# Optimization experiments

Measured on AMD Instinct MI355X. Metric: run time of the kernel, lower is better.

## Reference

```python
import jax, jax.numpy as jnp
import numpy as np
from jax import lax

IMG = 1280.0          # image side (80 * stride 16)
HF = WF = 80          # feature map
STRIDE = 16
A = 15                # anchors per location (5 sizes x 3 ratios)
KMIX = 5              # MDN mixture components
NIMG = 8
NGT = 32
PRE_NMS = 2000
POST_NMS = 1000
NMS_THRESH = 0.7
BATCH_PER_IMG = 256
POS_FRAC = 0.5
SCALE_CLAMP = float(np.log(1000.0 / 16.0))
LOG2PI = float(np.log(2.0 * np.pi))


def _make_anchors():
    sizes = np.array([32., 64., 128., 256., 512.])
    ratios = np.array([0.5, 1.0, 2.0])
    ws = (sizes[:, None] * np.sqrt(1.0 / ratios)[None, :]).reshape(-1)
    hs = (sizes[:, None] * np.sqrt(ratios)[None, :]).reshape(-1)
    base = np.stack([-ws / 2, -hs / 2, ws / 2, hs / 2], 1)  # [A,4]
    xs = (np.arange(WF) + 0.5) * STRIDE
    ys = (np.arange(HF) + 0.5) * STRIDE
    sx, sy = np.meshgrid(xs, ys)
    shifts = np.stack([sx.ravel(), sy.ravel(), sx.ravel(), sy.ravel()], 1)  # [HW,4]
    return jnp.asarray((shifts[:, None, :] + base[None]).reshape(-1, 4), jnp.float32)


def setup_inputs() -> dict:
    key = jax.random.key(0)
    k = jax.random.split(key, 6)
    R = HF * WF * A
    anchors = _make_anchors()                                                # [R,4]
    pi = jax.random.normal(k[0], (NIMG, KMIX, R), jnp.float32)
    mu = jax.random.normal(k[1], (NIMG, KMIX, R), jnp.float32)
    sigma = jax.random.uniform(k[2], (NIMG, KMIX, R), jnp.float32, 0.1, 1.0)
    deltas = jax.random.normal(k[3], (NIMG, R, 4), jnp.float32) * 0.1
    xy = jax.random.uniform(k[4], (NIMG, NGT, 2), jnp.float32, 0.0, 960.0)
    wh = jax.random.uniform(k[5], (NIMG, NGT, 2), jnp.float32, 20.0, 320.0)
    gt_boxes = jnp.concatenate([xy, xy + wh], -1)                            # [N,G,4]
    return {"anchors": anchors, "pi": pi, "mu": mu, "sigma": sigma,
            "deltas": deltas, "gt_boxes": gt_boxes}


def pairwise_iou(a, b):  # [M,4],[P,4] -> [M,P]
    area_a = (a[:, 2] - a[:, 0]) * (a[:, 3] - a[:, 1])
    area_b = (b[:, 2] - b[:, 0]) * (b[:, 3] - b[:, 1])
    lt = jnp.maximum(a[:, None, :2], b[None, :, :2])
    rb = jnp.minimum(a[:, None, 2:], b[None, :, 2:])
    wh = jnp.clip(rb - lt, 0.0)
    inter = wh[..., 0] * wh[..., 1]
    return inter / jnp.maximum(area_a[:, None] + area_b[None, :] - inter, 1e-9)


def apply_deltas(d, boxes):  # Box2BoxTransform.apply_deltas, weights=(1,1,1,1)
    w = boxes[:, 2] - boxes[:, 0]
    h = boxes[:, 3] - boxes[:, 1]
    cx = boxes[:, 0] + 0.5 * w
    cy = boxes[:, 1] + 0.5 * h
    dx, dy = d[:, 0], d[:, 1]
    dw = jnp.minimum(d[:, 2], SCALE_CLAMP)
    dh = jnp.minimum(d[:, 3], SCALE_CLAMP)
    pcx = dx * w + cx
    pcy = dy * h + cy
    pw = jnp.exp(dw) * w
    ph = jnp.exp(dh) * h
    return jnp.stack([pcx - 0.5 * pw, pcy - 0.5 * ph, pcx + 0.5 * pw, pcy + 0.5 * ph], 1)


def get_deltas(src, tgt):  # Box2BoxTransform.get_deltas
    sw = src[..., 2] - src[..., 0]
    sh = src[..., 3] - src[..., 1]
    scx = src[..., 0] + 0.5 * sw
    scy = src[..., 1] + 0.5 * sh
    tw = tgt[..., 2] - tgt[..., 0]
    th = tgt[..., 3] - tgt[..., 1]
    tcx = tgt[..., 0] + 0.5 * tw
    tcy = tgt[..., 1] + 0.5 * th
    return jnp.stack([(tcx - scx) / sw, (tcy - scy) / sh,
                      jnp.log(tw / sw), jnp.log(th / sh)], -1)


def _nms_image(boxes, scores, unc):  # [R,4],[R],[R,2] -> padded top proposals
    top_s, tidx = lax.top_k(scores, PRE_NMS)
    tb = jnp.clip(boxes[tidx], 0.0, IMG)   # clip to image
    tu = unc[tidx]
    iou = pairwise_iou(tb, tb)             # [PRE,PRE]
    ar = jnp.arange(PRE_NMS)

    def body(i, keep):
        sup = (iou[i] > NMS_THRESH) & (ar > i) & keep[i]
        return keep & ~sup

    keep = lax.fori_loop(0, PRE_NMS, body, jnp.ones((PRE_NMS,), bool))
    wv = tb[:, 2] - tb[:, 0]
    hv = tb[:, 3] - tb[:, 1]
    keep = keep & (wv > 0.0) & (hv > 0.0)  # min_box_size = 0
    ms = jnp.where(keep, top_s, -jnp.inf)
    out_s, oidx = lax.top_k(ms, POST_NMS)
    return tb[oidx], out_s, tu[oidx]


def _losses(anchors, pi, mu, sigma, deltas, gt_boxes):
    # label_and_sample_anchors (no_grad in torch)
    iou = lax.stop_gradient(jax.vmap(lambda g: pairwise_iou(g, anchors))(gt_boxes))  # [N,G,R]
    vals = iou.max(axis=1)                       # matched IoU quality  [N,R]
    idx = jnp.argmax(iou, axis=1)                # matched gt index     [N,R]
    labels = jnp.where(vals >= 0.7, 1, jnp.where(vals >= 0.3, -1, 0))
    best_gt = iou.max(axis=2)                    # [N,G]
    lq = jnp.any((iou >= best_gt[:, :, None] - 1e-7) & (best_gt[:, :, None] > 0), axis=1)
    labels = jnp.where(lq, 1, labels)            # allow_low_quality_matches
    # deterministic subsample to batch_size_per_image with positive_fraction
    pos = labels == 1
    neg = labels == 0
    n_pos = jnp.minimum(pos.sum(1), int(BATCH_PER_IMG * POS_FRAC))
    keep_pos = pos & (jnp.cumsum(pos, 1) <= n_pos[:, None])
    keep_neg = neg & (jnp.cumsum(neg, 1) <= (BATCH_PER_IMG - n_pos)[:, None])
    labels = jnp.where(keep_pos, 1, jnp.where(keep_neg, 0, -1))
    matched_gt = lax.stop_gradient(jax.vmap(lambda g, i: g[i])(gt_boxes, idx))  # [N,R,4]
    gt_deltas = get_deltas(lax.stop_gradient(anchors)[None], matched_gt)
    pos_mask = labels == 1
    # smooth_l1 with beta=0 -> L1, summed over positives
    loss_loc = jnp.sum(jnp.abs(deltas - gt_deltas) * pos_mask[..., None])
    valid = labels != -1
    t = jnp.clip(vals, 0.0, 1.0)
    lp = jax.nn.log_softmax(pi, axis=1)
    comp = lp - 0.5 * ((t[:, None, :] - mu) / sigma) ** 2 - jnp.log(sigma) - 0.5 * LOG2PI
    nll = -jax.nn.logsumexp(comp, axis=1)        # [N,R]
    loss_cls = jnp.sum(nll * valid)
    norm = BATCH_PER_IMG * pi.shape[0]
    return jnp.stack([loss_cls / norm, loss_loc / norm])


def reference(anchors, pi, mu, sigma, deltas, gt_boxes):
    # find_logit: pi-weighted mixture mean as objectness score
    pi_sm = jax.nn.softmax(pi, axis=1)           # [N,K,R]
    logits = jnp.sum(pi_sm * mu, axis=1)         # [N,R]
    # mdn_uncertainties: epistemic / aleatoric
    epis = jnp.sum(pi_sm * (mu - logits[:, None, :]) ** 2, axis=1)
    alea = jnp.sum(pi_sm * sigma ** 2, axis=1)
    unc = jnp.stack([epis, alea], -1)            # [N,R,2]
    # _decode_proposals
    boxes = jax.vmap(lambda d: apply_deltas(d, anchors))(deltas)  # [N,R,4]
    # find_top_rpn_proposals_uncertainty (pre-NMS topk, clip, NMS, post-NMS topk)
    prop_b, prop_s, prop_u = jax.vmap(_nms_image)(boxes, logits, unc)
    losses = _losses(anchors, pi, mu, sigma, deltas, gt_boxes)    # [loss_cls, loss_loc]
    return prop_b, prop_s, prop_u, losses
```

## Files before the change

### kernel.cpp

```cpp
#include <hip/hip_runtime.h>
#include <cstdint>
#include <cstddef>

typedef unsigned long long u64;
typedef unsigned int u32;
typedef unsigned short u16;
typedef unsigned char u8;

#define R_ANCH 96000
#define NIMG   8
#define KMIX   5
#define PRE    2000
#define POST   1000
#define NGT    32
#define NCHUNK 375
#define NBLK   48
#define MROW   2048
#define GC_STRIDE 16
#define SCAP   16
#define BIG_TH 64

#define IMG_SZ        1280.0f
#define NMS_T         0.7f
#define SCALE_CLAMP_F 4.135166556742356f
#define HALF_L2PI     0.9189385332046727f

__device__ __forceinline__ u64 make_key(float s, int r) {
  u32 u = __float_as_uint(s);
  u = (u & 0x80000000u) ? ~u : (u | 0x80000000u);
  return ((u64)u << 32) | (u64)(0xFFFFFFFFu - (u32)r);
}

__device__ __forceinline__ float dec_score(u64 key) {
  u32 o = (u32)(key >> 32);
  u32 bits = (o & 0x80000000u) ? (o ^ 0x80000000u) : ~o;
  return __uint_as_float(bits);
}

__device__ __forceinline__ float iou_pair(float a0,float a1,float a2,float a3,
                                          float b0,float b1,float b2,float b3) {
#pragma clang fp contract(off)
  float areaA = (a2-a0)*(a3-a1);
  float areaB = (b2-b0)*(b3-b1);
  float lx=fmaxf(a0,b0), ly=fmaxf(a1,b1);
  float rx=fminf(a2,b2), ry=fminf(a3,b3);
  float iw=fmaxf(rx-lx,0.0f), ih=fmaxf(ry-ly,0.0f);
  float inter=iw*ih;
  return inter / fmaxf(areaA+areaB-inter, 1e-9f);
}

__device__ __forceinline__ void pick2048(const u32* __restrict__ hist, int k,
                                         int* s_i, u32* s_u,
                                         int& d_out, int& k_out, u32& cnt_out) {
  int tid = threadIdx.x;
  int lane = tid & 63, w = tid >> 6;
  u32 h[8]; u32 ssum = 0;
#pragma unroll
  for (int i=0;i<8;++i){ h[i] = hist[2047 - (tid*8 + i)]; ssum += h[i]; }
  u32 incl = ssum;
  for (int off=1; off<64; off<<=1){
    u32 t = (u32)__shfl_up((int)incl, off, 64);
    if (lane >= off) incl += t;
  }
  if (lane==63) s_i[w] = (int)incl;
  __syncthreads();
  u32 base = 0;
  for (int ww=0; ww<w; ++ww) base += (u32)s_i[ww];
  u32 run = base + incl - ssum;
#pragma unroll
  for (int i=0;i<8;++i){
    u32 nr = run + h[i];
    if (run < (u32)k && nr >= (u32)k){
      s_u[0] = (u32)(2047 - (tid*8+i));
      s_u[1] = (u32)k - run;
      s_u[2] = h[i];
    }
    run = nr;
  }
  __syncthreads();
  d_out = (int)s_u[0]; k_out = (int)s_u[1]; cnt_out = s_u[2];
  __syncthreads();
}

__device__ __forceinline__ void scan2048_desc(const u32* __restrict__ h,
                                              u32* __restrict__ off,
                                              u32* __restrict__ wsum, int tid) {
  int b_hi = 2047 - 2*tid, b_lo = b_hi - 1;
  u32 h_hi = h[b_hi], h_lo = h[b_lo];
  u32 sum = h_hi + h_lo;
  u32 incl = sum;
  int lane = tid & 63, wv = tid >> 6;
  for (int o=1; o<64; o<<=1){
    u32 t = (u32)__shfl_up((int)incl, o, 64);
    if (lane >= o) incl += t;
  }
  if (lane==63) wsum[wv] = incl;
  __syncthreads();
  u32 base = 0;
  for (int w=0; w<wv; ++w) base += wsum[w];
  u32 excl = base + incl - sum;
  off[b_hi] = excl;
  off[b_lo] = excl + h_hi;
}

__global__ void kZero(u32* z, int nwords) {
  for (int i = blockIdx.x*256 + threadIdx.x; i < nwords; i += gridDim.x*256)
    z[i] = 0u;
}

__global__ __launch_bounds__(256) void kA_mdn(
    const float* __restrict__ pi, const float* __restrict__ mu,
    const float* __restrict__ sigma, float* __restrict__ logits,
    float* __restrict__ epis, float* __restrict__ alea,
    u32* __restrict__ hist0,
    const float* __restrict__ anchors, const float* __restrict__ gt,
    const float* __restrict__ deltas,
    float* __restrict__ nll_o, float* __restrict__ loc_o) {
  __shared__ u32 s_h[2048];
  __shared__ float s_gt[NGT*4];
  int tid = threadIdx.x;
  int r = blockIdx.x*256 + tid;
  int img = blockIdx.y;
  for (int b=tid; b<2048; b+=256) s_h[b]=0u;
  if (tid < NGT*4) s_gt[tid] = gt[img*NGT*4 + tid];
  size_t base = (size_t)img*KMIX*R_ANCH + r;
  float p[KMIX], m[KMIX], s[KMIX];
#pragma unroll
  for (int k=0;k<KMIX;k++){
    p[k]=pi[base+(size_t)k*R_ANCH];
    m[k]=mu[base+(size_t)k*R_ANCH];
    s[k]=sigma[base+(size_t)k*R_ANCH];
  }
  float mx = p[0];
#pragma unroll
  for (int k=1;k<KMIX;k++) mx = fmaxf(mx,p[k]);
  float e[KMIX]; float sum = 0.0f;
#pragma unroll
  for (int k=0;k<KMIX;k++){ e[k]=expf(p[k]-mx); sum += e[k]; }
  float w[KMIX]; float lg = 0.0f;
#pragma unroll
  for (int k=0;k<KMIX;k++){ w[k]=e[k]/sum; lg += w[k]*m[k]; }
  float ep = 0.0f, al = 0.0f;
#pragma unroll
  for (int k=0;k<KMIX;k++){ float d=m[k]-lg; ep += w[k]*d*d; al += w[k]*s[k]*s[k]; }
  size_t o = (size_t)img*R_ANCH + r;
  logits[o]=lg; epis[o]=ep; alea[o]=al;
  __syncthreads();
  u64 key = make_key(lg, r);
  atomicAdd(&s_h[(u32)(key>>53)], 1u);
  float4 a = ((const float4*)anchors)[r];
  float aA = (a.z-a.x)*(a.w-a.y);
  float bi = -1.0f, bu = 1.0f; int idx = 0;
#pragma unroll 4
  for (int g=0; g<NGT; ++g){
    float g0=s_gt[g*4], g1=s_gt[g*4+1], g2=s_gt[g*4+2], g3=s_gt[g*4+3];
    float ga=(g2-g0)*(g3-g1);
    float lx=fmaxf(g0,a.x), ly=fmaxf(g1,a.y);
    float rx=fminf(g2,a.z), ry=fminf(g3,a.w);
    float iw=fmaxf(rx-lx,0.0f), ih=fmaxf(ry-ly,0.0f);
    float inter=iw*ih;
    float uni = fmaxf(ga + aA - inter, 1e-9f);
    if (inter*bu > bi*uni){ bi=inter; bu=uni; idx=g; }
  }
  float vbest = bi/bu;
  float lsum = logf(sum);
  float t_ = fminf(fmaxf(vbest, 0.0f), 1.0f);
  float comp[KMIX];
#pragma unroll
  for (int k=0;k<KMIX;k++){
    float z = (t_ - m[k]) / s[k];
    comp[k] = (p[k]-mx-lsum) - 0.5f*z*z - logf(s[k]) - HALF_L2PI;
  }
  float cm = comp[0];
#pragma unroll
  for (int k=1;k<KMIX;k++) cm = fmaxf(cm, comp[k]);
  float se = 0.0f;
#pragma unroll
  for (int k=0;k<KMIX;k++) se += expf(comp[k]-cm);
  float nll = -(cm + logf(se));
  const float* gb = &s_gt[idx*4];
  float sw = a.z-a.x, sh = a.w-a.y;
  float scx = a.x+0.5f*sw, scy = a.y+0.5f*sh;
  float tw = gb[2]-gb[0], th = gb[3]-gb[1];
  float tcx = gb[0]+0.5f*tw, tcy = gb[1]+0.5f*th;
  float4 d = ((const float4*)deltas)[(size_t)img*R_ANCH + r];
  float loc = fabsf(d.x-(tcx-scx)/sw) + fabsf(d.y-(tcy-scy)/sh)
            + fabsf(d.z-logf(tw/sw)) + fabsf(d.w-logf(th/sh));
  nll_o[o] = nll; loc_o[o] = loc;
  __syncthreads();
  for (int b=tid; b<2048; b+=256){ u32 v=s_h[b]; if(v) atomicAdd(&hist0[img*2048+b], v); }
}

__global__ __launch_bounds__(256) void kL1_bestgt(const float* __restrict__ anchors,
                                                  const float* __restrict__ gt,
                                                  int* __restrict__ best) {
  __shared__ float s_gt[NGT*4];
  __shared__ float s_ga[NGT];
  __shared__ int s_best[NGT];
  int tid = threadIdx.x, img = blockIdx.y;
  if (tid < NGT*4) s_gt[tid] = gt[img*NGT*4 + tid];
  if (tid < NGT){
    const float* g4 = gt + img*NGT*4 + tid*4;
    s_ga[tid] = (g4[2]-g4[0])*(g4[3]-g4[1]);
    s_best[tid] = 0;
  }
  __syncthreads();
  float4 an[8]; float aA[8];
#pragma unroll
  for (int q=0; q<8; ++q){
    int r = blockIdx.x*256 + tid + q*(NBLK*256);
    an[q] = (r < R_ANCH) ? ((const float4*)anchors)[r]
                         : make_float4(0.f,0.f,0.f,0.f);
    aA[q] = (an[q].z-an[q].x)*(an[q].w-an[q].y);
  }
  float vmax[NGT];
#pragma unroll 2
  for (int g=0; g<NGT; ++g){
    float g0=s_gt[g*4], g1=s_gt[g*4+1], g2=s_gt[g*4+2], g3=s_gt[g*4+3];
    float ga=s_ga[g];
    float bi=0.0f, bu=1.0f;
#pragma unroll
    for (int q=0; q<8; ++q){
      float lx=fmaxf(g0,an[q].x), ly=fmaxf(g1,an[q].y);
      float rx=fminf(g2,an[q].z), ry=fminf(g3,an[q].w);
      float iw=fmaxf(rx-lx,0.0f), ih=fmaxf(ry-ly,0.0f);
      float inter=iw*ih;
      float uni=fmaxf(ga+aA[q]-inter,1e-9f);
      if (inter*bu > bi*uni){ bi=inter; bu=uni; }
    }
    vmax[g] = bi/bu;
  }
  int lane = tid & 63;
#pragma unroll
  for (int g=0; g<NGT; ++g){
    float v = vmax[g];
    v = fmaxf(v, __shfl_xor(v, 1, 64));
    v = fmaxf(v, __shfl_xor(v, 2, 64));
    v = fmaxf(v, __shfl_xor(v, 4, 64));
    v = fmaxf(v, __shfl_xor(v, 8, 64));
    v = fmaxf(v, __shfl_xor(v,16, 64));
    v = fmaxf(v, __shfl_xor(v,32, 64));
    if (lane==0 && v > 0.0f) atomicMax(&s_best[g], __float_as_int(v));
  }
  __syncthreads();
  if (tid < NGT) atomicMax(&best[img*NGT + tid], s_best[tid]);
}

__global__ __launch_bounds__(256) void kP1(const float* __restrict__ logits,
                                           const u32* __restrict__ hist0,
                                           u32* __restrict__ hist1) {
  __shared__ u32 s_h[2048];
  __shared__ int s_i[8]; __shared__ u32 s_u[3];
  int img = blockIdx.y, tid = threadIdx.x;
  int d0,k0; u32 c0;
  pick2048(hist0 + img*2048, PRE, s_i, s_u, d0,k0,c0);
  if (c0 <= 2048u) return;
  for (int b=tid; b<2048; b+=256) s_h[b]=0u;
  __syncthreads();
  const float* sc = logits + (size_t)img*R_ANCH;
  for (int r = blockIdx.x*256 + tid; r < R_ANCH; r += NBLK*256){
    u64 key = make_key(sc[r], r);
    if ((int)(key>>53) == d0) atomicAdd(&s_h[(u32)(key>>42)&2047u], 1u);
  }
  __syncthreads();
  for (int b=tid; b<2048; b+=256){ u32 v=s_h[b]; if(v) atomicAdd(&hist1[img*2048+b], v); }
}

__global__ __launch_bounds__(256) void kP2(const float* __restrict__ logits,
                                           const u32* __restrict__ hist0,
                                           const u32* __restrict__ hist1,
                                           u32* __restrict__ hist2) {
  __shared__ u32 s_h[2048];
  __shared__ int s_i[8]; __shared__ u32 s_u[3];
  int img = blockIdx.y, tid = threadIdx.x;
  int d0,k0; u32 c0;
  pick2048(hist0 + img*2048, PRE, s_i, s_u, d0,k0,c0);
  if (c0 <= 2048u) return;
  int d1,k1; u32 c1;
  pick2048(hist1 + img*2048, k0, s_i, s_u, d1,k1,c1);
  if (c1 <= 2048u) return;
  u64 p1 = ((u64)d0<<11) | (u64)d1;
  for (int b=tid; b<2048; b+=256) s_h[b]=0u;
  __syncthreads();
  const float* sc = logits + (size_t)img*R_ANCH;
  for (int r = blockIdx.x*256 + tid; r < R_ANCH; r += NBLK*256){
    u64 key = make_key(sc[r], r);
    if ((key>>42) == p1) atomicAdd(&s_h[(u32)(key>>31)&2047u], 1u);
  }
  __syncthreads();
  for (int b=tid; b<2048; b+=256){ u32 v=s_h[b]; if(v) atomicAdd(&hist2[img*2048+b], v); }
}

__global__ __launch_bounds__(256) void kGather(const float* __restrict__ logits,
    const u32* __restrict__ hist0, const u32* __restrict__ hist1,
    const u32* __restrict__ hist2, u64* __restrict__ cand, u32* __restrict__ gcnt) {
  __shared__ int s_i[8]; __shared__ u32 s_u[3];
  __shared__ u64 s_cand[2048];
  __shared__ u32 s_cnt, s_base;
  int img = blockIdx.y, tid = threadIdx.x;
  if (tid==0) s_cnt = 0u;
  int d,kk; u32 c;
  pick2048(hist0 + img*2048, PRE, s_i, s_u, d,kk,c);
  u64 p = (u64)d; int L = 0;
  if (c > 2048u){
    pick2048(hist1 + img*2048, kk, s_i, s_u, d,kk,c);
    p = (p<<11)|(u64)d; L = 1;
    if (c > 2048u){
      pick2048(hist2 + img*2048, kk, s_i, s_u, d,kk,c);
      p = (p<<11)|(u64)d; L = 2;
    }
  }
  u64 T = p << (64 - 11*(L+1));
  const float* sc = logits + (size_t)img*R_ANCH;
  int lane = tid & 63;
  for (int r = blockIdx.x*256 + tid; r < R_ANCH; r += NBLK*256){
    u64 key = make_key(sc[r], r);
    bool take = (key >= T);
    u64 b = __ballot(take);
    if (b){
      u32 base = 0;
      if (lane==0) base = atomicAdd(&s_cnt, (u32)__popcll(b));
      base = (u32)__shfl((int)base, 0, 64);
      if (take){
        u32 pos = base + (u32)__popcll(b & ((1ull<<lane)-1ull));
        if (pos < 2048u) s_cand[pos] = key;
        else {
          u32 gp = atomicAdd(&gcnt[img*GC_STRIDE], 1u);
          if (gp < 4096u) cand[(size_t)img*4096 + gp] = key;
        }
      }
    }
  }
  __syncthreads();
  u32 n = s_cnt < 2048u ? s_cnt : 2048u;
  if (tid==0) s_base = atomicAdd(&gcnt[img*GC_STRIDE], n);
  __syncthreads();
  u32 gb = s_base;
  for (u32 i=tid; i<n; i+=256)
    cand[(size_t)img*4096 + gb + i] = s_cand[i];
}

__global__ __launch_bounds__(1024) void kRank(
    const u64* __restrict__ cand, const u32* __restrict__ gcnt,
    const float* __restrict__ epis, const float* __restrict__ alea,
    const float* __restrict__ deltas, const float* __restrict__ anchors,
    float* __restrict__ tb, float* __restrict__ tu, float* __restrict__ ts) {
  __shared__ u64 s_key[4096];
  __shared__ u16 s_idx0[4096];
  __shared__ u16 s_idx1[4096];
  __shared__ u32 s_h0[2048];
  __shared__ u32 s_off0[2048];
  __shared__ u32 s_h1[2048];
  __shared__ u32 s_off1[2048];
  __shared__ u32 s_wsum[16];
  __shared__ u32 s_nbig;
  __shared__ u16 s_big[64];
  int tid = threadIdx.x, img = blockIdx.x;
  u32 cnt = gcnt[img*GC_STRIDE];
  if (cnt > 4096u) cnt = 4096u;
  const u64* cp = cand + (size_t)img*4096;
  for (int i=tid; i<4096; i+=1024) s_key[i] = (i < (int)cnt) ? cp[i] : 0ull;
  for (int b=tid; b<2048; b+=1024){ s_h0[b] = 0u; }
  if (tid==0) s_nbig = 0u;
  __syncthreads();
  for (int i=tid; i<(int)cnt; i+=1024)
    atomicAdd(&s_h0[(u32)(s_key[i]>>53)], 1u);
  __syncthreads();
  scan2048_desc(s_h0, s_off0, s_wsum, tid);
  __syncthreads();
  for (int b=tid; b<2048; b+=1024){
    u32 sz = s_h0[b];
    if (sz > BIG_TH && s_off0[b] < PRE){
      u32 q = atomicAdd(&s_nbig, 1u);
      if (q < 64u) s_big[q] = (u16)b;
    }
  }
  for (int i=tid; i<(int)cnt; i+=1024){
    u32 d = (u32)(s_key[i]>>53);
    u32 slot = atomicAdd(&s_off0[d], 1u);
    s_idx0[slot] = (u16)i;
  }
  __syncthreads();
  auto emit = [&](u64 my, u32 rank){
    if (rank < PRE){
      int p = (int)rank;
      u32 idx = 0xFFFFFFFFu - (u32)(my & 0xFFFFFFFFull);
      ts[img*PRE + p] = dec_score(my);
      float4 a = ((const float4*)anchors)[idx];
      float4 dd = ((const float4*)deltas)[(size_t)img*R_ANCH + idx];
      float w = a.z - a.x, h = a.w - a.y;
      float cx = a.x + 0.5f*w, cy = a.y + 0.5f*h;
      float dw = fminf(dd.z, SCALE_CLAMP_F), dh = fminf(dd.w, SCALE_CLAMP_F);
      float pcx = dd.x*w + cx, pcy = dd.y*h + cy;
      float pw = expf(dw)*w, ph = expf(dh)*h;
      float x0 = fminf(fmaxf(pcx - 0.5f*pw, 0.0f), IMG_SZ);
      float y0 = fminf(fmaxf(pcy - 0.5f*ph, 0.0f), IMG_SZ);
      float x1 = fminf(fmaxf(pcx + 0.5f*pw, 0.0f), IMG_SZ);
      float y1 = fminf(fmaxf(pcy + 0.5f*ph, 0.0f), IMG_SZ);
      ((float4*)tb)[(size_t)img*PRE + p] = make_float4(x0,y0,x1,y1);
      size_t o = (size_t)img*R_ANCH + idx;
      ((float2*)tu)[(size_t)img*PRE + p] = make_float2(epis[o], alea[o]);
    }
  };
  for (int i=tid; i<(int)cnt; i+=1024){
    u64 my = s_key[i];
    u32 d = (u32)(my>>53);
    u32 size = s_h0[d];
    if (size > BIG_TH) continue;
    u32 bs = s_off0[d] - size;
    if (bs >= PRE) continue;
    u32 rank = bs;
    for (u32 q=bs; q<bs+size; ++q)
      rank += (s_key[s_idx0[q]] > my) ? 1u : 0u;
    emit(my, rank);
  }
  __syncthreads();
  u32 nbig = s_nbig < 64u ? s_nbig : 64u;
  for (u32 bb=0; bb<nbig; ++bb){
    u32 B = s_big[bb];
    u32 size = s_h0[B];
    u32 base0 = s_off0[B] - size;
    for (int b=tid; b<2048; b+=1024) s_h1[b] = 0u;
    __syncthreads();
    for (u32 q=tid; q<size; q+=1024){
      u64 k = s_key[s_idx0[base0+q]];
      atomicAdd(&s_h1[(u32)(k>>42)&2047u], 1u);
    }
    __syncthreads();
    scan2048_desc(s_h1, s_off1, s_wsum, tid);
    __syncthreads();
    for (u32 q=tid; q<size; q+=1024){
      u16 ci = s_idx0[base0+q];
      u64 k = s_key[ci];
      u32 slot = atomicAdd(&s_off1[(u32)(k>>42)&2047u], 1u);
      s_idx1[slot] = ci;
    }
    __syncthreads();
    for (u32 q=tid; q<size; q+=1024){
      u16 ci = s_idx1[q];
      u64 my = s_key[ci];
      u32 d1 = (u32)(my>>42)&2047u;
      u32 ssz = s_h1[d1];
      u32 sbs = s_off1[d1] - ssz;
      u32 rank = base0 + sbs;
      for (u32 t2=sbs; t2<sbs+ssz; ++t2)
        rank += (s_key[s_idx1[t2]] > my) ? 1u : 0u;
      emit(my, rank);
    }
    __syncthreads();
  }
}

__global__ __launch_bounds__(1024) void kD_mask(const float* __restrict__ tb,
                                                u64* __restrict__ maskLT,
                                                u32* __restrict__ scnt,
                                                u16* __restrict__ slist) {
  __shared__ float4 s_tile[64];
  int tid = threadIdx.x;
  int a = blockIdx.x, img = blockIdx.y;
  const float4* tbi = (const float4*)tb + (size_t)img*PRE;
  if (tid < 64){
    int i = a*64 + tid;
    s_tile[tid] = (i < PRE) ? tbi[i] : make_float4(0.f,0.f,0.f,0.f);
  }
  __syncthreads();
  u64* outp = maskLT + ((size_t)img*32 + a)*MROW;
  u32* cnts = scnt + (size_t)img*2048;
  u16* lst  = slist + (size_t)img*2048*SCAP;
  int bmax = min(64, PRE - a*64);
  for (int j = a*64 + tid; j < MROW; j += 1024){
    u64 m = 0ull;
    if (j < PRE){
      float4 B = tbi[j];
      int blim = min(bmax, j - a*64);
      for (int b = 0; b < blim; ++b){
        float4 A = s_tile[b];
        float v = iou_pair(A.x,A.y,A.z,A.w, B.x,B.y,B.z,B.w);
        m |= (u64)(v > NMS_T) << b;
      }
    }
    outp[j] = m;
    u64 mm = m;
    while (mm){
      int b = __builtin_ctzll(mm); mm &= mm - 1ull;
      u32 slot = atomicAdd(&cnts[j], 1u);
      if (slot < SCAP) lst[(size_t)j*SCAP + slot] = (u16)(a*64 + b);
    }
  }
}

__global__ __launch_bounds__(1024) void kE_nms(const u64* __restrict__ maskLT,
                                               const u32* __restrict__ scnt,
                                               const u16* __restrict__ slist,
                                               u64* __restrict__ keep) {
  __shared__ u64 s_list64[2048*SCAP/4];
  __shared__ u16 s_cnt[2048];
  __shared__ u8  kbuf[2][2048];
  __shared__ u64 s_kw[32];
  __shared__ int s_change, s_ovf;
  int img = blockIdx.x, tid = threadIdx.x;
  const u64* gl = (const u64*)(slist + (size_t)img*2048*SCAP);
  for (int i=tid; i<2048*SCAP/4; i+=1024) s_list64[i] = gl[i];
  const u32* gc = scnt + (size_t)img*2048;
  for (int i=tid; i<2048; i+=1024) s_cnt[i] = (u16)gc[i];
  if (tid==0){ s_change = 0; s_ovf = 0; }
  __syncthreads();
  bool myovf = false;
#pragma unroll
  for (int q=0; q<2; ++q){
    int j = tid + q*1024;
    if (s_cnt[j] > SCAP) myovf = true;
    kbuf[0][j] = (j < PRE) ? 1 : 0;
  }
  if (myovf) s_ovf = 1;
  __syncthreads();
  const u64* MT = maskLT + (size_t)img*32*MROW;
  int cur = 0;
  for (int iter=0; iter<2048; ++iter){
    bool ovf = (s_ovf != 0);
    if (ovf && tid < 32){
      u64 w = 0ull;
      for (int b=0; b<64; ++b) w |= (u64)(kbuf[cur][tid*64+b] & 1) << b;
      s_kw[tid] = w;
    }
    __syncthreads();
    bool changed = false;
#pragma unroll
    for (int q=0; q<2; ++q){
      int j = tid + q*1024;
      u8 old = kbuf[cur][j];
      u8 nk = (j < PRE) ? 1 : 0;
      if (nk){
        int cnt = s_cnt[j];
        if (cnt <= SCAP){
          const u16* lp = (const u16*)&s_list64[j*(SCAP/4)];
          for (int i=0; i<cnt; ++i){
            if (kbuf[cur][lp[i]]){ nk = 0; break; }
          }
        } else {
          int amax = j >> 6;
          for (int a=0; a<=amax; ++a){
            if (MT[(size_t)a*MROW + j] & s_kw[a]){ nk = 0; break; }
          }
        }
      }
      kbuf[1-cur][j] = nk;
      changed |= (nk != old);
    }
    if (changed) s_change = 1;
    __syncthreads();
    int ch = s_change;
    __syncthreads();
    if (tid==0) s_change = 0;
    if (!ch) break;
    cur ^= 1;
  }
  if (tid < 32){
    u64 w = 0ull;
    for (int b=0; b<64; ++b) w |= (u64)(kbuf[cur][tid*64+b] & 1) << b;
    keep[img*32 + tid] = w;
  }
}

__global__ __launch_bounds__(256) void kL2_label(
    const float* __restrict__ anchors, const float* __restrict__ gt,
    const int* __restrict__ best,
    signed char* __restrict__ label, int* __restrict__ cpos, int* __restrict__ cneg) {
  __shared__ float s_gt[NGT*4];
  __shared__ float s_ga[NGT];
  __shared__ float s_bg[NGT];
  __shared__ int s_w[8];
  int tid = threadIdx.x, img = blockIdx.y;
  int r = blockIdx.x*256 + tid;
  if (tid < NGT*4) s_gt[tid] = gt[img*NGT*4 + tid];
  if (tid < NGT){
    const float* g4 = gt + img*NGT*4 + tid*4;
    s_ga[tid] = (g4[2]-g4[0])*(g4[3]-g4[1]);
    s_bg[tid] = __int_as_float(best[img*NGT + tid]);
  }
  __syncthreads();
  float4 a = ((const float4*)anchors)[r];
  float aA = (a.z-a.x)*(a.w-a.y);
  float bi=-1.0f, bu=1.0f; bool lq = false;
#pragma unroll 4
  for (int g=0; g<NGT; ++g){
    float g0=s_gt[g*4], g1=s_gt[g*4+1], g2=s_gt[g*4+2], g3=s_gt[g*4+3];
    float lx=fmaxf(g0,a.x), ly=fmaxf(g1,a.y);
    float rx=fminf(g2,a.z), ry=fminf(g3,a.w);
    float iw=fmaxf(rx-lx,0.0f), ih=fmaxf(ry-ly,0.0f);
    float inter=iw*ih;
    float uni = fmaxf(s_ga[g] + aA - inter, 1e-9f);
    if (inter*bu > bi*uni){ bi=inter; bu=uni; }
    float bg = s_bg[g];
    lq = lq || ((inter >= (bg - 1e-7f)*uni) && (bg > 0.0f));
  }
  float vbest = bi/bu;
  int lab = lq ? 1 : (vbest >= 0.7f ? 1 : (vbest >= 0.3f ? -1 : 0));
  label[(size_t)img*R_ANCH + r] = (signed char)lab;
  u64 bp = __ballot(lab==1), bn = __ballot(lab==0);
  int wid = tid>>6, lane = tid&63;
  if (lane==0){ s_w[wid*2]=__popcll(bp); s_w[wid*2+1]=__popcll(bn); }
  __syncthreads();
  if (tid==0){
    cpos[img*NCHUNK + blockIdx.x] = s_w[0]+s_w[2]+s_w[4]+s_w[6];
    cneg[img*NCHUNK + blockIdx.x] = s_w[1]+s_w[3]+s_w[5]+s_w[7];
  }
}

__global__ __launch_bounds__(512) void kL3_scan(const int* __restrict__ cpos,
                                                const int* __restrict__ cneg,
                                                int* __restrict__ opos,
                                                int* __restrict__ oneg,
                                                int* __restrict__ quota) {
  __shared__ int s_p[8], s_n[8];
  int img = blockIdx.x, tid = threadIdx.x;
  int vp=0, vn=0;
  if (tid < NCHUNK){ vp = cpos[img*NCHUNK+tid]; vn = cneg[img*NCHUNK+tid]; }
  int lane = tid&63, w = tid>>6;
  int ip=vp, in_=vn;
  for (int off=1; off<64; off<<=1){
    int tp=__shfl_up(ip,off,64), tn=__shfl_up(in_,off,64);
    if (lane>=off){ ip+=tp; in_+=tn; }
  }
  if (lane==63){ s_p[w]=ip; s_n[w]=in_; }
  __syncthreads();
  int bp=0,bn=0;
  for (int ww=0; ww<w; ++ww){ bp+=s_p[ww]; bn+=s_n[ww]; }
  if (tid < NCHUNK){
    opos[img*NCHUNK+tid] = bp+ip-vp;
    oneg[img*NCHUNK+tid] = bn+in_-vn;
  }
  if (tid==0){
    int tp=0,tn=0;
    for (int ww=0; ww<8; ++ww){ tp+=s_p[ww]; tn+=s_n[ww]; }
    int np = tp<128?tp:128;
    quota[img*2]=np; quota[img*2+1]=256-np;
  }
}

__global__ __launch_bounds__(256) void kL4_accum(
    const signed char* __restrict__ label, const float* __restrict__ nll_i,
    const float* __restrict__ loc_i, const int* __restrict__ opos,
    const int* __restrict__ oneg, const int* __restrict__ quota,
    float* __restrict__ acc) {
  __shared__ int s_wp[4], s_wn[4];
  __shared__ float s_red[8];
  int tid = threadIdx.x, img = blockIdx.y;
  int r = blockIdx.x*256 + tid;
  size_t o = (size_t)img*R_ANCH + r;
  int lab = label[o];
  bool pos = (lab==1), neg = (lab==0);
  u64 bp = __ballot(pos), bn = __ballot(neg);
  int wid = tid>>6, lane = tid&63;
  if (lane==0){ s_wp[wid]=__popcll(bp); s_wn[wid]=__popcll(bn); }
  __syncthreads();
  int pre_p = opos[img*NCHUNK + blockIdx.x];
  int pre_n = oneg[img*NCHUNK + blockIdx.x];
  for (int w=0; w<wid; ++w){ pre_p += s_wp[w]; pre_n += s_wn[w]; }
  u64 lm = (1ull<<lane) - 1ull;
  pre_p += __popcll(bp & lm);
  pre_n += __popcll(bn & lm);
  int np = quota[img*2], nn = quota[img*2+1];
  bool kp = pos && (pre_p < np);
  bool kn = neg && (pre_n < nn);
  float c_cls = (kp||kn) ? nll_i[o] : 0.0f;
  float c_loc = kp ? loc_i[o] : 0.0f;
  for (int of=32; of>0; of>>=1){
    c_cls += __shfl_down(c_cls, of, 64);
    c_loc += __shfl_down(c_loc, of, 64);
  }
  if (lane==0){ s_red[wid]=c_cls; s_red[4+wid]=c_loc; }
  __syncthreads();
  if (tid==0){
    float a = s_red[0]+s_red[1]+s_red[2]+s_red[3];
    float b = s_red[4]+s_red[5]+s_red[6]+s_red[7];
    if (a != 0.0f) atomicAdd(&acc[0], a);
    if (b != 0.0f) atomicAdd(&acc[1], b);
  }
}

__global__ __launch_bounds__(256) void kF_final(
    const float* __restrict__ tb, const float* __restrict__ tu,
    const float* __restrict__ ts, const u64* __restrict__ keepw,
    const float* __restrict__ acc, float* __restrict__ out) {
  __shared__ int s_wk[4], s_wn[4];
  __shared__ int s_kc, s_runk, s_runn;
  int tid = threadIdx.x, img = blockIdx.x;
  int wid = tid>>6, lane = tid&63;
  const u64* kw = keepw + img*32;
  const float NEG_INF = __uint_as_float(0xff800000u);
  int cnt = 0;
  for (int c=0; c<8; ++c){
    int p = c*256 + tid;
    float4 b = ((const float4*)tb)[(size_t)img*PRE + p];
    bool kp = (p < PRE) && (((kw[p>>6]>>(p&63))&1ull)!=0ull) && (b.z > b.x) && (b.w > b.y);
    cnt += kp ? 1 : 0;
  }
  for (int of=32; of>0; of>>=1) cnt += __shfl_down(cnt, of, 64);
  if (lane==0) s_wk[wid] = cnt;
  __syncthreads();
  if (tid==0){ s_kc = s_wk[0]+s_wk[1]+s_wk[2]+s_wk[3]; s_runk=0; s_runn=0; }
  __syncthreads();
  int kc = s_kc;
  for (int c=0; c<8; ++c){
    int p = c*256 + tid;
    float4 b = ((const float4*)tb)[(size_t)img*PRE + p];
    bool kp = (p < PRE) && (((kw[p>>6]>>(p&63))&1ull)!=0ull) && (b.z > b.x) && (b.w > b.y);
    u64 bk = __ballot(kp), bn = __ballot(!kp);
    if (lane==0){ s_wk[wid]=__popcll(bk); s_wn[wid]=__popcll(bn); }
    __syncthreads();
    int pk = s_runk, pn = s_runn;
    for (int w=0; w<wid; ++w){ pk += s_wk[w]; pn += s_wn[w]; }
    u64 lm = (1ull<<lane) - 1ull;
    pk += __popcll(bk & lm);
    pn += __popcll(bn & lm);
    int slot = kp ? pk : (kc + pn);
    if (slot < POST && p < PRE){
      ((float4*)out)[img*POST + slot] = b;
      out[32000 + img*POST + slot] = kp ? ts[img*PRE + p] : NEG_INF;
      ((float2*)(out + 40000))[img*POST + slot] = ((const float2*)tu)[(size_t)img*PRE + p];
    }
    __syncthreads();
    if (tid==0){
      s_runk += s_wk[0]+s_wk[1]+s_wk[2]+s_wk[3];
      s_runn += s_wn[0]+s_wn[1]+s_wn[2]+s_wn[3];
    }
    __syncthreads();
  }
  if (img==0 && tid<2) out[56000+tid] = acc[tid] * (1.0f/2048.0f);
}

extern "C" void kernel_launch(void* const* d_in, const int* in_sizes, int n_in,
                              void* d_out, int out_size, void* d_ws, size_t ws_size,
                              hipStream_t stream) {
  const float* anchors = (const float*)d_in[0];
  const float* pi      = (const float*)d_in[1];
  const float* mu      = (const float*)d_in[2];
  const float* sigma   = (const float*)d_in[3];
  const float* deltas  = (const float*)d_in[4];
  const float* gt      = (const float*)d_in[5];
  float* out = (float*)d_out;

  char* ws = (char*)d_ws;
  size_t off = 0;
  auto alloc = [&](size_t bytes) -> void* {
    void* p = (void*)(ws + off);
    off += (bytes + 255) & ~(size_t)255;
    return p;
  };
  float* logits = (float*)alloc((size_t)NIMG*R_ANCH*4);
  float* epis   = (float*)alloc((size_t)NIMG*R_ANCH*4);
  float* alea   = (float*)alloc((size_t)NIMG*R_ANCH*4);
  float* nll    = (float*)alloc((size_t)NIMG*R_ANCH*4);
  float* loc    = (float*)alloc((size_t)NIMG*R_ANCH*4);
  float* tb     = (float*)alloc((size_t)NIMG*PRE*4*4);
  float* tu     = (float*)alloc((size_t)NIMG*PRE*2*4);
  float* ts     = (float*)alloc((size_t)NIMG*PRE*4);
  u64*   maskLT = (u64*)  alloc((size_t)NIMG*32*MROW*8);
  u16*   slist  = (u16*)  alloc((size_t)NIMG*2048*SCAP*2);
  u64*   keepw  = (u64*)  alloc((size_t)NIMG*32*8);
  u64*   cand   = (u64*)  alloc((size_t)NIMG*4096*8);
  int*   cpos   = (int*)  alloc((size_t)NIMG*NCHUNK*4);
  int*   cneg   = (int*)  alloc((size_t)NIMG*NCHUNK*4);
  int*   opos   = (int*)  alloc((size_t)NIMG*NCHUNK*4);
  int*   oneg   = (int*)  alloc((size_t)NIMG*NCHUNK*4);
  int*   quota  = (int*)  alloc((size_t)NIMG*2*4);
  size_t zstart = off;
  u32*   hist0  = (u32*)  alloc((size_t)NIMG*2048*4);
  u32*   hist1  = (u32*)  alloc((size_t)NIMG*2048*4);
  u32*   hist2  = (u32*)  alloc((size_t)NIMG*2048*4);
  u32*   gcnt   = (u32*)  alloc((size_t)NIMG*GC_STRIDE*4);
  int*   best   = (int*)  alloc((size_t)NIMG*NGT*4);
  u32*   scnt   = (u32*)  alloc((size_t)NIMG*2048*4);
  float* acc    = (float*)alloc(8);
  int zwords = (int)((off - zstart) / 4);
  signed char* label = (signed char*)logits;

  kZero<<<dim3(64), dim3(256), 0, stream>>>((u32*)(ws + zstart), zwords);
  kA_mdn<<<dim3(NCHUNK, NIMG), dim3(256), 0, stream>>>(pi, mu, sigma, logits, epis, alea,
                                                       hist0, anchors, gt, deltas, nll, loc);
  kL1_bestgt<<<dim3(NBLK, NIMG), dim3(256), 0, stream>>>(anchors, gt, best);
  kP1<<<dim3(NBLK, NIMG), dim3(256), 0, stream>>>(logits, hist0, hist1);
  kP2<<<dim3(NBLK, NIMG), dim3(256), 0, stream>>>(logits, hist0, hist1, hist2);
  kGather<<<dim3(NBLK, NIMG), dim3(256), 0, stream>>>(logits, hist0, hist1, hist2, cand, gcnt);
  kRank<<<dim3(NIMG), dim3(1024), 0, stream>>>(cand, gcnt, epis, alea, deltas, anchors, tb, tu, ts);
  kD_mask<<<dim3(32, NIMG), dim3(1024), 0, stream>>>(tb, maskLT, scnt, slist);
  kE_nms<<<dim3(NIMG), dim3(1024), 0, stream>>>(maskLT, scnt, slist, keepw);
  kL2_label<<<dim3(NCHUNK, NIMG), dim3(256), 0, stream>>>(anchors, gt, best, label, cpos, cneg);
  kL3_scan<<<dim3(NIMG), dim3(512), 0, stream>>>(cpos, cneg, opos, oneg, quota);
  kL4_accum<<<dim3(NCHUNK, NIMG), dim3(256), 0, stream>>>(label, nll, loc, opos, oneg, quota, acc);
  kF_final<<<dim3(NIMG), dim3(256), 0, stream>>>(tb, tu, ts, keepw, acc, out);
}
```

Measured before the change: 284.4 us.

## Rank big histogram buckets per-wavefront in parallel and simplify mixture NLL math

In kRank, the big-bucket refinement used to run one bucket at a time across the whole 1024-thread block, with a 2048-bin histogram, a block-wide scan and several barriers per bucket. It now gives each of 16 wavefronts its own bucket, using a 256-bin sub-histogram over bits 45-52 and a wave-level shuffle scan, so up to 16 buckets are handled per round. The narrower 8-bit refinement leaves larger sub-buckets for the quadratic compare loop, which can cost more when a bucket is skewed. Separately, the per-anchor mixture NLL swaps the division for a hardware reciprocal and folds the log(sigma) terms into the exp-sum weights, so no logf calls are made per component.

```diff
diff --git a/kernel.cpp b/kernel.cpp
--- a/kernel.cpp
+++ b/kernel.cpp
@@ -165,19 +165,20 @@
   float vbest = bi/bu;
   float lsum = logf(sum);
   float t_ = fminf(fmaxf(vbest, 0.0f), 1.0f);
-  float comp[KMIX];
+  float cp[KMIX], rs[KMIX];
 #pragma unroll
   for (int k=0;k<KMIX;k++){
-    float z = (t_ - m[k]) / s[k];
-    comp[k] = (p[k]-mx-lsum) - 0.5f*z*z - logf(s[k]) - HALF_L2PI;
-  }
-  float cm = comp[0];
-#pragma unroll
-  for (int k=1;k<KMIX;k++) cm = fmaxf(cm, comp[k]);
+    rs[k] = __builtin_amdgcn_rcpf(s[k]);
+    float z = (t_ - m[k]) * rs[k];
+    cp[k] = (p[k]-mx-lsum) - 0.5f*z*z;
+  }
+  float cm = cp[0];
+#pragma unroll
+  for (int k=1;k<KMIX;k++) cm = fmaxf(cm, cp[k]);
   float se = 0.0f;
 #pragma unroll
-  for (int k=0;k<KMIX;k++) se += expf(comp[k]-cm);
-  float nll = -(cm + logf(se));
+  for (int k=0;k<KMIX;k++) se += expf(cp[k]-cm)*rs[k];
+  float nll = HALF_L2PI - cm - logf(se);
   const float* gb = &s_gt[idx*4];
   float sw = a.z-a.x, sh = a.w-a.y;
   float scx = a.x+0.5f*sw, scy = a.y+0.5f*sh;
@@ -350,8 +351,8 @@
   __shared__ u16 s_idx1[4096];
   __shared__ u32 s_h0[2048];
   __shared__ u32 s_off0[2048];
-  __shared__ u32 s_h1[2048];
-  __shared__ u32 s_off1[2048];
+  __shared__ u32 s_h8[16*256];
+  __shared__ u32 s_o8[16*256];
   __shared__ u32 s_wsum[16];
   __shared__ u32 s_nbig;
   __shared__ u16 s_big[64];
@@ -360,7 +361,7 @@
   if (cnt > 4096u) cnt = 4096u;
   const u64* cp = cand + (size_t)img*4096;
   for (int i=tid; i<4096; i+=1024) s_key[i] = (i < (int)cnt) ? cp[i] : 0ull;
-  for (int b=tid; b<2048; b+=1024){ s_h0[b] = 0u; }
+  for (int b=tid; b<2048; b+=1024) s_h0[b] = 0u;
   if (tid==0) s_nbig = 0u;
   __syncthreads();
   for (int i=tid; i<(int)cnt; i+=1024)
@@ -416,36 +417,62 @@
   }
   __syncthreads();
   u32 nbig = s_nbig < 64u ? s_nbig : 64u;
-  for (u32 bb=0; bb<nbig; ++bb){
-    u32 B = s_big[bb];
-    u32 size = s_h0[B];
-    u32 base0 = s_off0[B] - size;
-    for (int b=tid; b<2048; b+=1024) s_h1[b] = 0u;
-    __syncthreads();
-    for (u32 q=tid; q<size; q+=1024){
-      u64 k = s_key[s_idx0[base0+q]];
-      atomicAdd(&s_h1[(u32)(k>>42)&2047u], 1u);
-    }
-    __syncthreads();
-    scan2048_desc(s_h1, s_off1, s_wsum, tid);
-    __syncthreads();
-    for (u32 q=tid; q<size; q+=1024){
-      u16 ci = s_idx0[base0+q];
-      u64 k = s_key[ci];
-      u32 slot = atomicAdd(&s_off1[(u32)(k>>42)&2047u], 1u);
-      s_idx1[slot] = ci;
-    }
-    __syncthreads();
-    for (u32 q=tid; q<size; q+=1024){
-      u16 ci = s_idx1[q];
-      u64 my = s_key[ci];
-      u32 d1 = (u32)(my>>42)&2047u;
-      u32 ssz = s_h1[d1];
-      u32 sbs = s_off1[d1] - ssz;
-      u32 rank = base0 + sbs;
-      for (u32 t2=sbs; t2<sbs+ssz; ++t2)
-        rank += (s_key[s_idx1[t2]] > my) ? 1u : 0u;
-      emit(my, rank);
+  int wv = tid>>6, lane = tid&63;
+  u32* h8 = &s_h8[wv*256];
+  u32* o8 = &s_o8[wv*256];
+  for (u32 bb0=0; bb0<nbig; bb0+=16){
+    u32 bb = bb0 + (u32)wv;
+    bool active = (bb < nbig);
+    u32 B=0, size=0, base0=0;
+    if (active){ B = s_big[bb]; size = s_h0[B]; base0 = s_off0[B] - size; }
+    for (int b=lane; b<256; b+=64) h8[b] = 0u;
+    __syncthreads();
+    if (active){
+      for (u32 q=lane; q<size; q+=64){
+        u64 k = s_key[s_idx0[base0+q]];
+        atomicAdd(&h8[(u32)(k>>45)&255u], 1u);
+      }
+    }
+    __syncthreads();
+    u32 hb0=0,hb1=0,hb2=0,hb3=0,ssum=0;
+    if (active){
+      hb0=h8[255-4*lane]; hb1=h8[254-4*lane];
+      hb2=h8[253-4*lane]; hb3=h8[252-4*lane];
+      ssum=hb0+hb1+hb2+hb3;
+    }
+    u32 incl=ssum;
+    for (int o=1;o<64;o<<=1){
+      u32 t=(u32)__shfl_up((int)incl,o,64);
+      if (lane>=o) incl+=t;
+    }
+    u32 run = incl - ssum;
+    if (active){
+      o8[255-4*lane]=run; run+=hb0;
+      o8[254-4*lane]=run; run+=hb1;
+      o8[253-4*lane]=run; run+=hb2;
+      o8[252-4*lane]=run;
+    }
+    __syncthreads();
+    if (active){
+      for (u32 q=lane; q<size; q+=64){
+        u16 ci = s_idx0[base0+q];
+        u32 slot = atomicAdd(&o8[(u32)(s_key[ci]>>45)&255u], 1u);
+        s_idx1[base0+slot] = ci;
+      }
+    }
+    __syncthreads();
+    if (active){
+      for (u32 q=lane; q<size; q+=64){
+        u16 ci = s_idx1[base0+q];
+        u64 my = s_key[ci];
+        u32 d8 = (u32)(my>>45)&255u;
+        u32 ssz = h8[d8];
+        u32 sbs = o8[d8]-ssz;
+        u32 rank = base0 + sbs;
+        for (u32 t2=sbs; t2<sbs+ssz; ++t2)
+          rank += (s_key[s_idx1[base0+t2]] > my) ? 1u:0u;
+        emit(my, rank);
+      }
     }
     __syncthreads();
   }
```

Measured after the change: 289.6 us. No clear change (+1.8%).
